# Kernel optimization log

Measured on AMD Instinct MI355X. Metric: run time of the kernel, lower is better.

## Reference

```python
import jax, jax.numpy as jnp
import numpy as np

DIM = 768
NUM_HEADS = 12
HEAD_DIM = DIM // NUM_HEADS
SCALE = HEAD_DIM ** -0.5


def setup_inputs() -> dict:
    key = jax.random.key(0)
    ks = jax.random.split(key, 7)
    B, N = 4, 2048
    s = DIM ** -0.5
    return {
        "x": jax.random.normal(ks[0], (B, N, DIM), dtype=jnp.float32),
        "attn_bias": jax.random.normal(ks[1], (1, NUM_HEADS, N, N), dtype=jnp.float32),
        "Wq": jax.random.normal(ks[2], (DIM, DIM), dtype=jnp.float32) * s,
        "Wk": jax.random.normal(ks[3], (DIM, DIM), dtype=jnp.float32) * s,
        "Wv": jax.random.normal(ks[4], (DIM, DIM), dtype=jnp.float32) * s,
        "Wp": jax.random.normal(ks[5], (DIM, DIM), dtype=jnp.float32) * s,
        "bp": jax.random.normal(ks[6], (DIM,), dtype=jnp.float32) * 0.02,
    }


def reference(x, attn_bias, Wq, Wk, Wv, Wp, bp):
    B, N, C = x.shape
    # Linear layers use y = x @ W.T (torch convention); split heads: [B,H,N,D]
    def heads(y):
        return y.reshape(B, N, NUM_HEADS, HEAD_DIM).transpose(0, 2, 1, 3)
    q = heads(x @ Wq.T)
    k = heads(x @ Wk.T)
    v = heads(x @ Wv.T)
    attn = jnp.einsum("bhnd,bhmd->bhnm", q, k) * SCALE + attn_bias
    attn = jax.nn.softmax(attn, axis=-1)
    out = jnp.einsum("bhnm,bhmd->bhnd", attn, v)
    out = out.transpose(0, 2, 1, 3).reshape(B, N, C)
    return out @ Wp.T + bp
```

## Files before the change

### kernel.cpp

```cpp
#include <hip/hip_runtime.h>
#include <hip/hip_bf16.h>

#define NTOK 2048
#define NHEADS 12
#define HDIM 64
#define DIM 768
#define BATCH 4
#define SC2_    0.18033688011112042f
#define LOG2E_  1.4426950408889634f
#define SHIFT2_ 23.083120654223415f

typedef __attribute__((ext_vector_type(8))) short short8;
typedef __attribute__((ext_vector_type(4))) float f32x4;
typedef __attribute__((ext_vector_type(16))) float f32x16;

__device__ __forceinline__ short f2bf(float f) {
  union { float f; unsigned u; } v; v.f = f;
  unsigned r = v.u + 0x7fffu + ((v.u >> 16) & 1u);
  return (short)(r >> 16);
}

__device__ __forceinline__ f32x4 mfma_bf16(short8 a, short8 b, f32x4 c) {
  return __builtin_amdgcn_mfma_f32_16x16x32_bf16(a, b, c, 0, 0, 0);
}

__device__ __forceinline__ f32x16 mfma32(short8 a, short8 b, f32x16 c) {
  return __builtin_amdgcn_mfma_f32_32x32x16_bf16(a, b, c, 0, 0, 0);
}

__device__ __forceinline__ void gload_lds16(const void* g, void* l) {
  __builtin_amdgcn_global_load_lds((const __attribute__((address_space(1))) void*)g,
                                   (__attribute__((address_space(3))) void*)l, 16, 0, 0);
}

__device__ __forceinline__ float exp2_hw(float x) {
  float r; asm("v_exp_f32 %0, %1" : "=v"(r) : "v"(x)); return r;
}

__device__ __forceinline__ unsigned cvt_pk_bf16(float lo, float hi) {
  unsigned r; asm("v_cvt_pk_bf16_f32 %0, %1, %2" : "=v"(r) : "v"(lo), "v"(hi)); return r;
}

__device__ __forceinline__ int swz(int r) { return (r ^ (r >> 3)) & 7; }

__global__ void cvt_x(const float* __restrict__ src, short* __restrict__ dst) {
  int i = blockIdx.x * 256 + threadIdx.x;
  float4 v = ((const float4*)src)[i];
  short4 o; o.x = f2bf(v.x); o.y = f2bf(v.y); o.z = f2bf(v.z); o.w = f2bf(v.w);
  ((short4*)dst)[i] = o;
}

__global__ void cvt_w(const float* __restrict__ w0, const float* __restrict__ w1,
                      const float* __restrict__ w2, const float* __restrict__ w3,
                      short* __restrict__ d0, short* __restrict__ d1,
                      short* __restrict__ d2, short* __restrict__ d3) {
  int i = blockIdx.x * 256 + threadIdx.x;
  const float* s = blockIdx.y == 0 ? w0 : blockIdx.y == 1 ? w1 : blockIdx.y == 2 ? w2 : w3;
  short* d = blockIdx.y == 0 ? d0 : blockIdx.y == 1 ? d1 : blockIdx.y == 2 ? d2 : d3;
  float4 v = ((const float4*)s)[i];
  short4 o; o.x = f2bf(v.x); o.y = f2bf(v.y); o.z = f2bf(v.z); o.w = f2bf(v.w);
  ((short4*)d)[i] = o;
}

__device__ __forceinline__ void gemm_mainloop(const short* __restrict__ A,
                                              const short* __restrict__ B,
                                              int mbase, int nbase,
                                              short* As, short* Bs,
                                              f32x4 (&acc)[4][4], int lane, int w) {
  int lr = lane & 15, lg = lane >> 4;
  int wr = w >> 1, wc = w & 1;
  for (int kb = 0; kb < DIM; kb += 64) {
    if (kb) __syncthreads();
#pragma unroll
    for (int c = 0; c < 4; ++c) {
      int row = w * 32 + c * 8 + (lane >> 3);
      int sch = (lane & 7) ^ (row & 7);
      gload_lds16(A + (size_t)(mbase + row) * DIM + kb + sch * 8, (char*)As + w * 4096 + c * 1024);
      gload_lds16(B + (size_t)(nbase + row) * DIM + kb + sch * 8, (char*)Bs + w * 4096 + c * 1024);
    }
    __syncthreads();
#pragma unroll
    for (int ks = 0; ks < 2; ++ks) {
      short8 af[4], bf[4];
#pragma unroll
      for (int i = 0; i < 4; ++i) {
        int row = wr * 64 + i * 16 + lr;
        int ch = (ks * 4 + lg) ^ (row & 7);
        af[i] = *(const short8*)(As + row * 64 + ch * 8);
      }
#pragma unroll
      for (int j = 0; j < 4; ++j) {
        int row = wc * 64 + j * 16 + lr;
        int ch = (ks * 4 + lg) ^ (row & 7);
        bf[j] = *(const short8*)(Bs + row * 64 + ch * 8);
      }
#pragma unroll
      for (int i = 0; i < 4; ++i)
#pragma unroll
        for (int j = 0; j < 4; ++j)
          acc[i][j] = mfma_bf16(af[i], bf[j], acc[i][j]);
    }
  }
}

__global__ __launch_bounds__(256, 2) void gemm_qkv(const short* __restrict__ xb,
    const short* __restrict__ wq, const short* __restrict__ wk, const short* __restrict__ wv,
    short* __restrict__ Qh, short* __restrict__ Kh, short* __restrict__ Vt) {
  __shared__ __align__(16) short As[128 * 64];
  __shared__ __align__(16) short Bs[128 * 64];
  int nt = blockIdx.x, mt = blockIdx.y, z = blockIdx.z;
  const short* B = z == 0 ? wq : (z == 1 ? wk : wv);
  int tid = threadIdx.x, lane = tid & 63, w = tid >> 6;
  f32x4 acc[4][4] = {};
  gemm_mainloop(xb, B, mt * 128, nt * 128, As, Bs, acc, lane, w);
  int lr = lane & 15, lg = lane >> 4, wr = w >> 1, wc = w & 1;
  if (z < 2) {
    short* dst = z == 0 ? Qh : Kh;
#pragma unroll
    for (int i = 0; i < 4; ++i)
#pragma unroll
      for (int j = 0; j < 4; ++j) {
        int m = mt * 128 + wr * 64 + i * 16 + lg * 4;
        int n = nt * 128 + wc * 64 + j * 16 + lr;
        int bb = m >> 11, nn = m & 2047, hh = n >> 6, d = n & 63;
        size_t base = (((size_t)bb * NHEADS + hh) * NTOK + nn) * HDIM + d;
#pragma unroll
        for (int r = 0; r < 4; ++r)
          dst[base + (size_t)r * HDIM] = f2bf(acc[i][j][r]);
      }
  } else {
#pragma unroll
    for (int i = 0; i < 4; ++i)
#pragma unroll
      for (int j = 0; j < 4; ++j) {
        int m = mt * 128 + wr * 64 + i * 16 + lg * 4;
        int n = nt * 128 + wc * 64 + j * 16 + lr;
        int bb = m >> 11, nn = m & 2047, hh = n >> 6, d = n & 63;
        short4 pk;
        pk.x = f2bf(acc[i][j][0]); pk.y = f2bf(acc[i][j][1]);
        pk.z = f2bf(acc[i][j][2]); pk.w = f2bf(acc[i][j][3]);
        *(short4*)(Vt + (((size_t)bb * NHEADS + hh) * HDIM + d) * NTOK + nn) = pk;
      }
  }
}

__global__ __launch_bounds__(256, 3) void attn_fused(const short* __restrict__ Qh,
    const short* __restrict__ Kh, const short* __restrict__ Vt,
    const float* __restrict__ bias, short* __restrict__ Ob) {
  __shared__ __align__(16) short Ks[2][32 * 64];
  __shared__ __align__(16) short Vs[2][32 * 64];
  __shared__ __align__(16) float Bs[2][128 * 32];
  int d0 = blockIdx.x;
  int wg = (d0 & 7) * 96 + (d0 >> 3);
  int b = wg & 3, qb = (wg >> 2) & 15, h = wg >> 6;
  int tid = threadIdx.x, lane = tid & 63, w = tid >> 6;
  int ql = lane & 31, hi = lane >> 5;

  const short* Q = Qh + ((size_t)b * NHEADS + h) * NTOK * HDIM;
  const short* K = Kh + ((size_t)b * NHEADS + h) * NTOK * HDIM;
  const short* V = Vt + ((size_t)b * NHEADS + h) * HDIM * NTOK;
  int qrow = qb * 128 + w * 32 + ql;
  const float* Bg = bias + ((size_t)h * NTOK + qb * 128) * NTOK;

  short8 qf[4];
#pragma unroll
  for (int i = 0; i < 4; ++i)
    qf[i] = *(const short8*)(Q + (size_t)qrow * HDIM + i * 16 + hi * 8);

  float psum = 0.f;
  f32x16 oacc0 = {}, oacc1 = {};

  int l8 = lane >> 3, s7 = lane & 7;

#define STAGE_ALL(BUF, KV)                                                     \
  {                                                                            \
       \
    int krow = w * 8 + l8;                                                     \
    gload_lds16(K + (size_t)(KV + krow) * HDIM + ((s7 ^ swz(krow)) * 8),       \
                (char*)Ks[BUF] + w * 1024);                                    \
                   \
    int vrp = w * 8 + l8;                                                      \
    int vu = s7 ^ swz(vrp);                                                    \
    gload_lds16(V + (size_t)(vrp * 2 + (vu >> 2)) * NTOK + (KV) + (vu & 3) * 8,\
                (char*)Vs[BUF] + w * 1024);                                    \
                                      \
    _Pragma("unroll")                                                          \
    for (int j = 0; j < 4; ++j) {                                              \
      int brow = w * 32 + j * 8 + l8;                                          \
      gload_lds16(Bg + (size_t)brow * NTOK + (KV) + ((s7 ^ swz(brow)) * 4),    \
                  (char*)Bs[BUF] + w * 4096 + j * 1024);                       \
    }                                                                          \
  }

  STAGE_ALL(0, 0)
  __syncthreads();

  for (int t = 0; t < NTOK / 32; ++t) {
    int cur = t & 1;
    int kv = t * 32;
    if (t < NTOK / 32 - 1) STAGE_ALL(cur ^ 1, kv + 32)

    f32x16 sacc = {};
    __builtin_amdgcn_s_setprio(1);
#pragma unroll
    for (int i = 0; i < 4; ++i) {
      short8 kf = *(const short8*)(Ks[cur] + ql * 64 + (((i * 2 + hi) ^ swz(ql)) * 8));
      sacc = mfma32(kf, qf[i], sacc);
    }
    __builtin_amdgcn_s_setprio(0);

    f32x4 bvr[4];
    int brow = w * 32 + ql;
#pragma unroll
    for (int g = 0; g < 4; ++g)
      bvr[g] = *(const f32x4*)(Bs[cur] + brow * 32 + (((g * 2 + hi) ^ swz(brow)) * 4));

    float p[16];
#pragma unroll
    for (int rg = 0; rg < 16; ++rg) {
      float tb = fmaf(bvr[rg >> 2][rg & 3], LOG2E_, -SHIFT2_);
      p[rg] = exp2_hw(fmaf(sacc[rg], SC2_, tb));
    }
    float ts = 0.f;
#pragma unroll
    for (int g = 0; g < 4; ++g)
      ts += (p[g * 4] + p[g * 4 + 1]) + (p[g * 4 + 2] + p[g * 4 + 3]);
    psum += ts;

    unsigned Wd[4][2];
#pragma unroll
    for (int g = 0; g < 4; ++g) {
      Wd[g][0] = cvt_pk_bf16(p[g * 4], p[g * 4 + 1]);
      Wd[g][1] = cvt_pk_bf16(p[g * 4 + 2], p[g * 4 + 3]);
    }

#pragma unroll
    for (int cc = 0; cc < 2; ++cc) {
      auto r0 = __builtin_amdgcn_permlane32_swap(Wd[cc * 2][0], Wd[cc * 2 + 1][0], false, false);
      auto r1 = __builtin_amdgcn_permlane32_swap(Wd[cc * 2][1], Wd[cc * 2 + 1][1], false, false);
      union { unsigned u[4]; short8 s; } pb;
      pb.u[0] = r0[0]; pb.u[1] = r1[0]; pb.u[2] = r0[1]; pb.u[3] = r1[1];
      __builtin_amdgcn_s_setprio(1);
      {
        int rp0 = (ql >> 1);
        int s0 = (((ql & 1) * 4 + cc * 2 + hi) ^ swz(rp0));
        short8 vf0 = *(const short8*)(Vs[cur] + rp0 * 64 + s0 * 8);
        oacc0 = mfma32(vf0, pb.s, oacc0);
        int rp1 = 16 + (ql >> 1);
        int s1 = (((ql & 1) * 4 + cc * 2 + hi) ^ swz(rp1));
        short8 vf1 = *(const short8*)(Vs[cur] + rp1 * 64 + s1 * 8);
        oacc1 = mfma32(vf1, pb.s, oacc1);
      }
      __builtin_amdgcn_s_setprio(0);
    }

    __syncthreads();
  }
#undef STAGE_ALL

  float fs = psum + __shfl_xor(psum, 32);
  float inv = 1.f / fs;
  size_t obase = ((size_t)b * NTOK + qrow) * DIM + h * HDIM;
#pragma unroll
  for (int g = 0; g < 4; ++g) {
    unsigned u0 = cvt_pk_bf16(oacc0[g * 4] * inv, oacc0[g * 4 + 1] * inv);
    unsigned u1 = cvt_pk_bf16(oacc0[g * 4 + 2] * inv, oacc0[g * 4 + 3] * inv);
    uint2 pk0; pk0.x = u0; pk0.y = u1;
    *(uint2*)(Ob + obase + g * 8 + hi * 4) = pk0;
    unsigned u2 = cvt_pk_bf16(oacc1[g * 4] * inv, oacc1[g * 4 + 1] * inv);
    unsigned u3 = cvt_pk_bf16(oacc1[g * 4 + 2] * inv, oacc1[g * 4 + 3] * inv);
    uint2 pk1; pk1.x = u2; pk1.y = u3;
    *(uint2*)(Ob + obase + 32 + g * 8 + hi * 4) = pk1;
  }
}

__global__ __launch_bounds__(256, 2) void gemm_proj(const short* __restrict__ Ob,
    const short* __restrict__ wp, const float* __restrict__ bp, float* __restrict__ out) {
  __shared__ __align__(16) short As[128 * 64];
  __shared__ __align__(16) short Bs[128 * 64];
  int nt = blockIdx.x, mt = blockIdx.y;
  int tid = threadIdx.x, lane = tid & 63, w = tid >> 6;
  f32x4 acc[4][4] = {};
  gemm_mainloop(Ob, wp, mt * 128, nt * 128, As, Bs, acc, lane, w);
  int lr = lane & 15, lg = lane >> 4, wr = w >> 1, wc = w & 1;
#pragma unroll
  for (int j = 0; j < 4; ++j) {
    int n = nt * 128 + wc * 64 + j * 16 + lr;
    float bpv = bp[n];
#pragma unroll
    for (int i = 0; i < 4; ++i) {
      int m = mt * 128 + wr * 64 + i * 16 + lg * 4;
#pragma unroll
      for (int r = 0; r < 4; ++r)
        out[(size_t)(m + r) * DIM + n] = acc[i][j][r] + bpv;
    }
  }
}

extern "C" void kernel_launch(void* const* d_in, const int* in_sizes, int n_in,
                              void* d_out, int out_size, void* d_ws, size_t ws_size,
                              hipStream_t stream) {
  const float* x    = (const float*)d_in[0];
  const float* bias = (const float*)d_in[1];
  const float* Wq   = (const float*)d_in[2];
  const float* Wk   = (const float*)d_in[3];
  const float* Wv   = (const float*)d_in[4];
  const float* Wp   = (const float*)d_in[5];
  const float* bp   = (const float*)d_in[6];
  float* out = (float*)d_out;

  char* ws = (char*)d_ws;
  short* xb  = (short*)(ws);
  short* wqb = (short*)(ws + 12582912);
  short* wkb = (short*)(ws + 13762560);
  short* wvb = (short*)(ws + 14942208);
  short* wpb = (short*)(ws + 16121856);
  short* Qh  = (short*)(ws + 17301504);
  short* Kh  = (short*)(ws + 29884416);
  short* Vt  = (short*)(ws + 42467328);
  short* Ob  = (short*)(ws + 55050240);

  cvt_x<<<6144, 256, 0, stream>>>(x, xb);
  cvt_w<<<dim3(576, 4), 256, 0, stream>>>(Wq, Wk, Wv, Wp, wqb, wkb, wvb, wpb);
  gemm_qkv<<<dim3(6, 64, 3), 256, 0, stream>>>(xb, wqb, wkb, wvb, Qh, Kh, Vt);
  attn_fused<<<768, 256, 0, stream>>>(Qh, Kh, Vt, bias, Ob);
  gemm_proj<<<dim3(6, 64), 256, 0, stream>>>(Ob, wpb, bp, out);
}
```

Before: 191.4 us.

## Triple-buffer K/V/bias staging with partial vmcnt waits in attention loop

Moves the fused attention kernel from double to triple buffering of the K, V and bias tiles in LDS, keeping two tiles in flight. Each iteration now waits only until the oldest tile has landed (vmcnt(6)) before a raw barrier, where it previously drained everything through __syncthreads. This is meant to hide more global-load latency, mainly from the large fp32 bias stream. In exchange LDS use per block grows and occupancy drops from 3 to 2 blocks per CU in the launch bounds. The hand-written vmcnt counts also depend on the exact number of loads issued per stage.

```diff
diff --git a/kernel.cpp b/kernel.cpp
--- a/kernel.cpp
+++ b/kernel.cpp
@@ -144,12 +144,12 @@
   }
 }
 
-__global__ __launch_bounds__(256, 3) void attn_fused(const short* __restrict__ Qh,
+__global__ __launch_bounds__(256, 2) void attn_fused(const short* __restrict__ Qh,
     const short* __restrict__ Kh, const short* __restrict__ Vt,
     const float* __restrict__ bias, short* __restrict__ Ob) {
-  __shared__ __align__(16) short Ks[2][32 * 64];
-  __shared__ __align__(16) short Vs[2][32 * 64];
-  __shared__ __align__(16) float Bs[2][128 * 32];
+  __shared__ __align__(16) short Ks[3][32 * 64];
+  __shared__ __align__(16) short Vs[3][32 * 64];
+  __shared__ __align__(16) float Bs[3][128 * 32];
   int d0 = blockIdx.x;
   int wg = (d0 & 7) * 96 + (d0 >> 3);
   int b = wg & 3, qb = (wg >> 2) & 15, h = wg >> 6;
@@ -174,16 +174,13 @@
 
 #define STAGE_ALL(BUF, KV)                                                     \
   {                                                                            \
-       \
     int krow = w * 8 + l8;                                                     \
-    gload_lds16(K + (size_t)(KV + krow) * HDIM + ((s7 ^ swz(krow)) * 8),       \
+    gload_lds16(K + (size_t)((KV) + krow) * HDIM + ((s7 ^ swz(krow)) * 8),     \
                 (char*)Ks[BUF] + w * 1024);                                    \
-                   \
     int vrp = w * 8 + l8;                                                      \
     int vu = s7 ^ swz(vrp);                                                    \
     gload_lds16(V + (size_t)(vrp * 2 + (vu >> 2)) * NTOK + (KV) + (vu & 3) * 8,\
                 (char*)Vs[BUF] + w * 1024);                                    \
-                                      \
     _Pragma("unroll")                                                          \
     for (int j = 0; j < 4; ++j) {                                              \
       int brow = w * 32 + j * 8 + l8;                                          \
@@ -193,18 +190,25 @@
   }
 
   STAGE_ALL(0, 0)
-  __syncthreads();
+  STAGE_ALL(1, 32)
+  asm volatile("s_waitcnt vmcnt(6)" ::: "memory");
+  __builtin_amdgcn_s_barrier();
+  __builtin_amdgcn_sched_barrier(0);
 
   for (int t = 0; t < NTOK / 32; ++t) {
-    int cur = t & 1;
+    int cur = t % 3;
     int kv = t * 32;
-    if (t < NTOK / 32 - 1) STAGE_ALL(cur ^ 1, kv + 32)
+    if (t < NTOK / 32 - 2) STAGE_ALL((t + 2) % 3, kv + 64)
+
+    const short* Kc = Ks[cur];
+    const short* Vc = Vs[cur];
+    const float* Bc = Bs[cur];
 
     f32x16 sacc = {};
     __builtin_amdgcn_s_setprio(1);
 #pragma unroll
     for (int i = 0; i < 4; ++i) {
-      short8 kf = *(const short8*)(Ks[cur] + ql * 64 + (((i * 2 + hi) ^ swz(ql)) * 8));
+      short8 kf = *(const short8*)(Kc + ql * 64 + (((i * 2 + hi) ^ swz(ql)) * 8));
       sacc = mfma32(kf, qf[i], sacc);
     }
     __builtin_amdgcn_s_setprio(0);
@@ -213,7 +217,7 @@
     int brow = w * 32 + ql;
 #pragma unroll
     for (int g = 0; g < 4; ++g)
-      bvr[g] = *(const f32x4*)(Bs[cur] + brow * 32 + (((g * 2 + hi) ^ swz(brow)) * 4));
+      bvr[g] = *(const f32x4*)(Bc + brow * 32 + (((g * 2 + hi) ^ swz(brow)) * 4));
 
     float p[16];
 #pragma unroll
@@ -244,17 +248,24 @@
       {
         int rp0 = (ql >> 1);
         int s0 = (((ql & 1) * 4 + cc * 2 + hi) ^ swz(rp0));
-        short8 vf0 = *(const short8*)(Vs[cur] + rp0 * 64 + s0 * 8);
+        short8 vf0 = *(const short8*)(Vc + rp0 * 64 + s0 * 8);
         oacc0 = mfma32(vf0, pb.s, oacc0);
         int rp1 = 16 + (ql >> 1);
         int s1 = (((ql & 1) * 4 + cc * 2 + hi) ^ swz(rp1));
-        short8 vf1 = *(const short8*)(Vs[cur] + rp1 * 64 + s1 * 8);
+        short8 vf1 = *(const short8*)(Vc + rp1 * 64 + s1 * 8);
         oacc1 = mfma32(vf1, pb.s, oacc1);
       }
       __builtin_amdgcn_s_setprio(0);
     }
 
-    __syncthreads();
+    if (t < NTOK / 32 - 1) {
+      if (t < NTOK / 32 - 2)
+        asm volatile("s_waitcnt vmcnt(6)" ::: "memory");
+      else
+        asm volatile("s_waitcnt vmcnt(0)" ::: "memory");
+      __builtin_amdgcn_s_barrier();
+      __builtin_amdgcn_sched_barrier(0);
+    }
   }
 #undef STAGE_ALL
 
```

Result: slower. 245.7 us (+28.3%).
